# Optimization experiments

Hardware: AMD Instinct MI355X
Metric: run time of the kernel (lower is better)

Reference implementation:

```python
import jax, jax.numpy as jnp
import numpy as np

N = 262144        # 64^3 grid unknowns
NNZ = 7 * N       # ~7-point stencil sparsity
BS = 32


def setup_inputs() -> dict:
    key = jax.random.key(0)
    k1, k2, k3, k4, k5 = jax.random.split(key, 5)
    y_pred = jax.random.normal(k1, (BS, N), dtype=jnp.float32)
    y_true = jax.random.normal(k2, (BS, N), dtype=jnp.float32)
    A_vals = jax.random.normal(k3, (NNZ,), dtype=jnp.float32)
    A_rows = jax.random.randint(k4, (NNZ,), 0, N, dtype=jnp.int32)
    A_cols = jax.random.randint(k5, (NNZ,), 0, N, dtype=jnp.int32)
    return {"y_pred": y_pred, "y_true": y_true, "A_vals": A_vals,
            "A_rows": A_rows, "A_cols": A_cols}


def reference(y_pred, y_true, A_vals, A_rows, A_cols):
    # YhatY[b] = <y_true[b], y_pred[b]>
    YhatY = jnp.sum(y_true * y_pred, axis=1)                      # (bs,)
    # Sparse matvec per batch: YhatAt = (A @ y_pred.T).T, COO form.
    # gathered[e, b] = A_vals[e] * y_pred[b, A_cols[e]]
    gathered = (y_pred[:, A_cols] * A_vals).T                     # (nnz, bs)
    YhatAt = jax.ops.segment_sum(gathered, A_rows, num_segments=N).T  # (bs, N)
    # YhatYhatAt[b] = <y_pred[b], A y_pred[b]>
    YhatYhatAt = jnp.sum(y_pred * YhatAt, axis=1)                 # (bs,)
    # diag(YhatY / YhatYhatAt) @ YhatAt == row-wise scale by alpha
    alpha = YhatY / YhatYhatAt                                    # (bs,)
    resid = y_true - alpha[:, None] * YhatAt                      # (bs, N)
    return jnp.mean(jnp.sum(resid * resid, axis=1))
```

## Files before the change

kernel.cpp:

```cpp
#include <hip/hip_runtime.h>

#define NGRID 262144
#define NNZ_C 1835008
#define TP    260


__global__ __launch_bounds__(256) void k_prep(
        const float* __restrict__ yp, const float* __restrict__ yt,
        float* __restrict__ yp_t, float* __restrict__ yt_t,
        float* __restrict__ yat_t) {
    __shared__ __align__(16) float T[32 * TP];
    const int tid = threadIdx.x;
    const int l = tid & 63, w = tid >> 6;
    const int fam = blockIdx.x >> 10;
    const size_t n0 = (size_t)(blockIdx.x & 1023) * 256;
    const float* src = fam ? yt : yp;
    #pragma unroll
    for (int s = 0; s < 8; ++s) {
        const int b = s * 4 + w;
        const float4 a = *(const float4*)(src + (size_t)b * NGRID + n0 + 4 * l);
        *(float4*)(&T[b * TP + 4 * l]) = a;
    }
    __syncthreads();
    float4* dst4 = (float4*)((fam ? yt_t : yp_t) + n0 * 32);
    float4* yat4 = (float4*)(yat_t + n0 * 32);
    #pragma unroll
    for (int q = 0; q < 8; ++q) {
        const int f = q * 256 + tid;
        const int n = f >> 3;
        const int bb = 4 * (f & 7);
        float4 v;
        v.x = T[(bb + 0) * TP + n];
        v.y = T[(bb + 1) * TP + n];
        v.z = T[(bb + 2) * TP + n];
        v.w = T[(bb + 3) * TP + n];
        dst4[f] = v;
        if (!fam) yat4[f] = make_float4(0.f, 0.f, 0.f, 0.f);
    }
}

__global__ void k_scatter(const float* __restrict__ vals,
                          const int* __restrict__ rows,
                          const int* __restrict__ cols,
                          const float* __restrict__ yp_t,
                          float* __restrict__ yat_t) {
    const size_t tid = (size_t)blockIdx.x * blockDim.x + threadIdx.x;
    const int b = (int)(tid & 31);
    const size_t e = tid >> 5;
    const float v = vals[e];
    const int r = rows[e];
    const int c = cols[e];
    const float x = yp_t[(size_t)c * 32 + b];
    atomicAdd(&yat_t[(size_t)r * 32 + b], v * x);
}

__global__ __launch_bounds__(256) void k_post(
        const float* __restrict__ yat_t, const float* __restrict__ yp_t,
        const float* __restrict__ yt_t, float* __restrict__ p2) {
    __shared__ float redA[5][1024];
    const int tid = threadIdx.x;
    const size_t base = (size_t)blockIdx.x * 1024;
    const float4* yat4 = (const float4*)yat_t;
    const float4* yp4 = (const float4*)yp_t;
    const float4* yt4 = (const float4*)yt_t;
    float c1[4] = {0,0,0,0}, c2[4] = {0,0,0,0}, c3[4] = {0,0,0,0};
    float tt[4] = {0,0,0,0}, sy[4] = {0,0,0,0};
    #pragma unroll
    for (int q = 0; q < 4; ++q) {
        const size_t f = base + q * 256 + tid;
        const float4 a = yat4[f];
        const float4 p = yp4[f];
        const float4 t = yt4[f];
        c1[0] = fmaf(p.x, a.x, c1[0]); c2[0] = fmaf(t.x, a.x, c2[0]);
        c3[0] = fmaf(a.x, a.x, c3[0]); tt[0] = fmaf(t.x, t.x, tt[0]);
        sy[0] = fmaf(t.x, p.x, sy[0]);
        c1[1] = fmaf(p.y, a.y, c1[1]); c2[1] = fmaf(t.y, a.y, c2[1]);
        c3[1] = fmaf(a.y, a.y, c3[1]); tt[1] = fmaf(t.y, t.y, tt[1]);
        sy[1] = fmaf(t.y, p.y, sy[1]);
        c1[2] = fmaf(p.z, a.z, c1[2]); c2[2] = fmaf(t.z, a.z, c2[2]);
        c3[2] = fmaf(a.z, a.z, c3[2]); tt[2] = fmaf(t.z, t.z, tt[2]);
        sy[2] = fmaf(t.z, p.z, sy[2]);
        c1[3] = fmaf(p.w, a.w, c1[3]); c2[3] = fmaf(t.w, a.w, c2[3]);
        c3[3] = fmaf(a.w, a.w, c3[3]); tt[3] = fmaf(t.w, t.w, tt[3]);
        sy[3] = fmaf(t.w, p.w, sy[3]);
    }
    #pragma unroll
    for (int k = 0; k < 4; ++k) {
        redA[0][4 * tid + k] = c1[k];
        redA[1][4 * tid + k] = c2[k];
        redA[2][4 * tid + k] = c3[k];
        redA[3][4 * tid + k] = tt[k];
        redA[4][4 * tid + k] = sy[k];
    }
    __syncthreads();
    if (tid < 32) {
        #pragma unroll
        for (int s = 0; s < 5; ++s) {
            float acc = 0.f;
            #pragma unroll
            for (int j = 0; j < 32; ++j) acc += redA[s][tid + 32 * j];
            p2[blockIdx.x * 160 + s * 32 + tid] = acc;
        }
    }
}

__global__ __launch_bounds__(256) void k_finish1(
        const float* __restrict__ p2, float* __restrict__ pr2) {
    const int tid = threadIdx.x, g = blockIdx.x;
    if (tid < 160) {
        float acc = 0.f;
        #pragma unroll
        for (int j = 0; j < 32; ++j) acc += p2[(size_t)(g * 32 + j) * 160 + tid];
        pr2[g * 160 + tid] = acc;
    }
}

__global__ __launch_bounds__(256) void k_finish2(
        const float* __restrict__ pr2, float* __restrict__ out) {
    __shared__ float tot[160];
    __shared__ float lb[32];
    const int tid = threadIdx.x;
    if (tid < 160) {
        float acc = 0.f;
        #pragma unroll
        for (int j = 0; j < 64; ++j) acc += pr2[j * 160 + tid];
        tot[tid] = acc;
    }
    __syncthreads();
    if (tid < 32) {
        const float c1 = tot[0 + tid];
        const float c2 = tot[32 + tid];
        const float c3 = tot[64 + tid];
        const float stt = tot[96 + tid];
        const float sty = tot[128 + tid];
        const float a = sty / c1;
        lb[tid] = fmaf(a * a, c3, fmaf(-2.f * a, c2, stt));
    }
    __syncthreads();
    if (tid == 0) {
        float s = 0.f;
        #pragma unroll
        for (int i = 0; i < 32; ++i) s += lb[i];
        out[0] = s * (1.0f / 32.0f);
    }
}

extern "C" void kernel_launch(void* const* d_in, const int* in_sizes, int n_in,
                              void* d_out, int out_size, void* d_ws, size_t ws_size,
                              hipStream_t stream) {
    const float* yp = (const float*)d_in[0];
    const float* yt = (const float*)d_in[1];
    const float* Av = (const float*)d_in[2];
    const int*   Ar = (const int*)d_in[3];
    const int*   Ac = (const int*)d_in[4];
    float* out = (float*)d_out;

    float* ws    = (float*)d_ws;
    float* yp_t  = ws;
    float* yat_t = yp_t + (size_t)NGRID * 32;
    float* yt_t  = yat_t + (size_t)NGRID * 32;
    float* p2    = yt_t + (size_t)NGRID * 32;
    float* pr2   = p2 + 2048 * 160;

    k_prep<<<2048, 256, 0, stream>>>(yp, yt, yp_t, yt_t, yat_t);
    k_scatter<<<(NNZ_C * 32) / 256, 256, 0, stream>>>(Av, Ar, Ac, yp_t, yat_t);
    k_post<<<2048, 256, 0, stream>>>(yat_t, yp_t, yt_t, p2);
    k_finish1<<<64, 256, 0, stream>>>(p2, pr2);
    k_finish2<<<1, 256, 0, stream>>>(pr2, out);
}
```

Before: 330.7 us.

## Replace atomic COO scatter with per-call CSR build and row-gather SpMM

Each call now converts the COO matrix to CSR with a two-pass bucket sort: a coarse 1024-bucket histogram, scan and reorder, then a per-bucket sort into rows. A gather kernel then computes each row's sparse product for all 32 batches without atomics and fuses the dot-product reductions. This removes the yat_t buffer, its zeroing, and the 58M global float atomics. In exchange it adds several sorting kernels with atomics on the cursor and in shared memory, and a serial single-block scan. The gather loop is latency-bound, with two lanes per batch per row.

Result: slower. 360.3 us (+9.0%).

```diff
diff --git a/kernel.cpp b/kernel.cpp
--- a/kernel.cpp
+++ b/kernel.cpp
@@ -2,18 +2,23 @@
 
 #define NGRID 262144
 #define NNZ_C 1835008
+#define NBKT  1024
 #define TP    260
 
 
 __global__ __launch_bounds__(256) void k_prep(
         const float* __restrict__ yp, const float* __restrict__ yt,
         float* __restrict__ yp_t, float* __restrict__ yt_t,
-        float* __restrict__ yat_t) {
+        int* __restrict__ hist) {
     __shared__ __align__(16) float T[32 * TP];
     const int tid = threadIdx.x;
     const int l = tid & 63, w = tid >> 6;
     const int fam = blockIdx.x >> 10;
     const size_t n0 = (size_t)(blockIdx.x & 1023) * 256;
+    if (blockIdx.x == 0) {
+        #pragma unroll
+        for (int i = 0; i < 4; ++i) hist[i * 256 + tid] = 0;
+    }
     const float* src = fam ? yt : yp;
     #pragma unroll
     for (int s = 0; s < 8; ++s) {
@@ -23,7 +28,6 @@
     }
     __syncthreads();
     float4* dst4 = (float4*)((fam ? yt_t : yp_t) + n0 * 32);
-    float4* yat4 = (float4*)(yat_t + n0 * 32);
     #pragma unroll
     for (int q = 0; q < 8; ++q) {
         const int f = q * 256 + tid;
@@ -35,72 +39,149 @@
         v.z = T[(bb + 2) * TP + n];
         v.w = T[(bb + 3) * TP + n];
         dst4[f] = v;
-        if (!fam) yat4[f] = make_float4(0.f, 0.f, 0.f, 0.f);
-    }
-}
-
-__global__ void k_scatter(const float* __restrict__ vals,
-                          const int* __restrict__ rows,
-                          const int* __restrict__ cols,
-                          const float* __restrict__ yp_t,
-                          float* __restrict__ yat_t) {
-    const size_t tid = (size_t)blockIdx.x * blockDim.x + threadIdx.x;
-    const int b = (int)(tid & 31);
-    const size_t e = tid >> 5;
-    const float v = vals[e];
-    const int r = rows[e];
-    const int c = cols[e];
-    const float x = yp_t[(size_t)c * 32 + b];
-    atomicAdd(&yat_t[(size_t)r * 32 + b], v * x);
-}
-
-__global__ __launch_bounds__(256) void k_post(
-        const float* __restrict__ yat_t, const float* __restrict__ yp_t,
+    }
+}
+
+__global__ __launch_bounds__(256) void k_hist(const int* __restrict__ rows,
+                                              int* __restrict__ hist) {
+    __shared__ int h[NBKT];
+    const int tid = threadIdx.x;
+    for (int i = tid; i < NBKT; i += 256) h[i] = 0;
+    __syncthreads();
+    const int chunk = NNZ_C / 512;
+    const size_t e0 = (size_t)blockIdx.x * chunk;
+    for (int i = tid; i < chunk; i += 256) atomicAdd(&h[rows[e0 + i] >> 8], 1);
+    __syncthreads();
+    for (int i = tid; i < NBKT; i += 256)
+        if (h[i]) atomicAdd(&hist[i], h[i]);
+}
+
+__global__ __launch_bounds__(1024) void k_scan(const int* __restrict__ hist,
+                                               int* __restrict__ base,
+                                               int* __restrict__ cursor) {
+    __shared__ int s[2][NBKT];
+    const int tid = threadIdx.x;
+    const int v = hist[tid];
+    s[0][tid] = v;
+    __syncthreads();
+    int p = 0;
+    for (int off = 1; off < NBKT; off <<= 1) {
+        int t = s[p][tid];
+        if (tid >= off) t += s[p][tid - off];
+        s[1 ^ p][tid] = t;
+        __syncthreads();
+        p ^= 1;
+    }
+    const int excl = s[p][tid] - v;
+    base[tid] = excl;
+    cursor[tid] = excl;
+    if (tid == 0) base[NBKT] = NNZ_C;
+}
+
+__global__ __launch_bounds__(256) void k_reorder(
+        const int* __restrict__ rows, const int* __restrict__ cols,
+        const float* __restrict__ vals, int* __restrict__ cursor,
+        int* __restrict__ rc_out, float* __restrict__ v_out) {
+    __shared__ int h[NBKT];
+    __shared__ int bl[NBKT];
+    const int tid = threadIdx.x;
+    for (int i = tid; i < NBKT; i += 256) h[i] = 0;
+    __syncthreads();
+    const int chunk = NNZ_C / 256;
+    const size_t e0 = (size_t)blockIdx.x * chunk;
+    for (int i = tid; i < chunk; i += 256) atomicAdd(&h[rows[e0 + i] >> 8], 1);
+    __syncthreads();
+    for (int i = tid; i < NBKT; i += 256) {
+        const int c = h[i];
+        bl[i] = c ? atomicAdd(&cursor[i], c) : 0;
+        h[i] = 0;
+    }
+    __syncthreads();
+    for (int i = tid; i < chunk; i += 256) {
+        const int r = rows[e0 + i];
+        const int bk = r >> 8;
+        const int off = atomicAdd(&h[bk], 1);
+        const int pos = bl[bk] + off;
+        rc_out[pos] = ((r & 255) << 24) | cols[e0 + i];
+        v_out[pos] = vals[e0 + i];
+    }
+}
+
+__global__ __launch_bounds__(256) void k_reorder2(
+        const int* __restrict__ rc1, const float* __restrict__ v1,
+        const int* __restrict__ base, int* __restrict__ cols_s,
+        float* __restrict__ vals_s, int* __restrict__ row_ptr) {
+    __shared__ int s[2][256];
+    __shared__ int cur[256];
+    const int tid = threadIdx.x;
+    const int k = blockIdx.x;
+    const int start = base[k], end = base[k + 1];
+    s[0][tid] = 0;
+    __syncthreads();
+    for (int i = start + tid; i < end; i += 256)
+        atomicAdd(&s[0][((unsigned)rc1[i]) >> 24], 1);
+    __syncthreads();
+    const int v = s[0][tid];
+    int p = 0;
+    for (int off = 1; off < 256; off <<= 1) {
+        int t = s[p][tid];
+        if (tid >= off) t += s[p][tid - off];
+        s[1 ^ p][tid] = t;
+        __syncthreads();
+        p ^= 1;
+    }
+    const int excl = s[p][tid] - v;
+    row_ptr[k * 256 + tid] = start + excl;
+    cur[tid] = excl;
+    __syncthreads();
+    for (int i = start + tid; i < end; i += 256) {
+        const int rc = rc1[i];
+        const int r8 = (int)(((unsigned)rc) >> 24);
+        const int off = atomicAdd(&cur[r8], 1);
+        cols_s[start + off] = rc & 0x3FFFF;
+        vals_s[start + off] = v1[i];
+    }
+    if (k == NBKT - 1 && tid == 0) row_ptr[NGRID] = NNZ_C;
+}
+
+__global__ __launch_bounds__(256) void k_gather(
+        const int* __restrict__ cols_s, const float* __restrict__ vals_s,
+        const int* __restrict__ row_ptr, const float* __restrict__ yp_t,
         const float* __restrict__ yt_t, float* __restrict__ p2) {
-    __shared__ float redA[5][1024];
-    const int tid = threadIdx.x;
-    const size_t base = (size_t)blockIdx.x * 1024;
-    const float4* yat4 = (const float4*)yat_t;
-    const float4* yp4 = (const float4*)yp_t;
-    const float4* yt4 = (const float4*)yt_t;
-    float c1[4] = {0,0,0,0}, c2[4] = {0,0,0,0}, c3[4] = {0,0,0,0};
-    float tt[4] = {0,0,0,0}, sy[4] = {0,0,0,0};
-    #pragma unroll
-    for (int q = 0; q < 4; ++q) {
-        const size_t f = base + q * 256 + tid;
-        const float4 a = yat4[f];
-        const float4 p = yp4[f];
-        const float4 t = yt4[f];
-        c1[0] = fmaf(p.x, a.x, c1[0]); c2[0] = fmaf(t.x, a.x, c2[0]);
-        c3[0] = fmaf(a.x, a.x, c3[0]); tt[0] = fmaf(t.x, t.x, tt[0]);
-        sy[0] = fmaf(t.x, p.x, sy[0]);
-        c1[1] = fmaf(p.y, a.y, c1[1]); c2[1] = fmaf(t.y, a.y, c2[1]);
-        c3[1] = fmaf(a.y, a.y, c3[1]); tt[1] = fmaf(t.y, t.y, tt[1]);
-        sy[1] = fmaf(t.y, p.y, sy[1]);
-        c1[2] = fmaf(p.z, a.z, c1[2]); c2[2] = fmaf(t.z, a.z, c2[2]);
-        c3[2] = fmaf(a.z, a.z, c3[2]); tt[2] = fmaf(t.z, t.z, tt[2]);
-        sy[2] = fmaf(t.z, p.z, sy[2]);
-        c1[3] = fmaf(p.w, a.w, c1[3]); c2[3] = fmaf(t.w, a.w, c2[3]);
-        c3[3] = fmaf(a.w, a.w, c3[3]); tt[3] = fmaf(t.w, t.w, tt[3]);
-        sy[3] = fmaf(t.w, p.w, sy[3]);
-    }
-    #pragma unroll
-    for (int k = 0; k < 4; ++k) {
-        redA[0][4 * tid + k] = c1[k];
-        redA[1][4 * tid + k] = c2[k];
-        redA[2][4 * tid + k] = c3[k];
-        redA[3][4 * tid + k] = tt[k];
-        redA[4][4 * tid + k] = sy[k];
-    }
-    __syncthreads();
-    if (tid < 32) {
-        #pragma unroll
-        for (int s = 0; s < 5; ++s) {
-            float acc = 0.f;
-            #pragma unroll
-            for (int j = 0; j < 32; ++j) acc += redA[s][tid + 32 * j];
-            p2[blockIdx.x * 160 + s * 32 + tid] = acc;
+    __shared__ float R[4][5][32];
+    const int tid = threadIdx.x;
+    const int l = tid & 63, w = tid >> 6;
+    const int b = l & 31, j = l >> 5;
+    float C1 = 0.f, C2 = 0.f, C3 = 0.f, TT = 0.f, SY = 0.f;
+    const int r0 = blockIdx.x * 64 + w * 16;
+    for (int i = 0; i < 16; ++i) {
+        const int r = r0 + i;
+        const int s = row_ptr[r], e = row_ptr[r + 1];
+        float acc = 0.f;
+        for (int idx = s + j; idx < e; idx += 2) {
+            const int c = cols_s[idx];
+            const float v = vals_s[idx];
+            acc = fmaf(v, yp_t[(size_t)c * 32 + b], acc);
         }
+        acc += __shfl_down(acc, 32);
+        const float ypr = yp_t[(size_t)r * 32 + b];
+        const float ytr = yt_t[(size_t)r * 32 + b];
+        if (j == 0) {
+            C1 = fmaf(acc, ypr, C1);
+            C2 = fmaf(acc, ytr, C2);
+            C3 = fmaf(acc, acc, C3);
+        } else {
+            TT = fmaf(ytr, ytr, TT);
+            SY = fmaf(ytr, ypr, SY);
+        }
+    }
+    if (j == 0) { R[w][0][b] = C1; R[w][1][b] = C2; R[w][2][b] = C3; }
+    else        { R[w][3][b] = TT; R[w][4][b] = SY; }
+    __syncthreads();
+    if (tid < 160) {
+        const int s5 = tid >> 5, bb = tid & 31;
+        p2[blockIdx.x * 160 + tid] =
+            R[0][s5][bb] + R[1][s5][bb] + R[2][s5][bb] + R[3][s5][bb];
     }
 }
 
@@ -110,7 +191,7 @@
     if (tid < 160) {
         float acc = 0.f;
         #pragma unroll
-        for (int j = 0; j < 32; ++j) acc += p2[(size_t)(g * 32 + j) * 160 + tid];
+        for (int j = 0; j < 64; ++j) acc += p2[(size_t)(g * 64 + j) * 160 + tid];
         pr2[g * 160 + tid] = acc;
     }
 }
@@ -155,16 +236,26 @@
     const int*   Ac = (const int*)d_in[4];
     float* out = (float*)d_out;
 
-    float* ws    = (float*)d_ws;
-    float* yp_t  = ws;
-    float* yat_t = yp_t + (size_t)NGRID * 32;
-    float* yt_t  = yat_t + (size_t)NGRID * 32;
-    float* p2    = yt_t + (size_t)NGRID * 32;
-    float* pr2   = p2 + 2048 * 160;
-
-    k_prep<<<2048, 256, 0, stream>>>(yp, yt, yp_t, yt_t, yat_t);
-    k_scatter<<<(NNZ_C * 32) / 256, 256, 0, stream>>>(Av, Ar, Ac, yp_t, yat_t);
-    k_post<<<2048, 256, 0, stream>>>(yat_t, yp_t, yt_t, p2);
+    float* ws     = (float*)d_ws;
+    float* yp_t   = ws;
+    float* yt_t   = yp_t + (size_t)NGRID * 32;
+    int*   rc1    = (int*)(yt_t + (size_t)NGRID * 32);
+    float* v1     = (float*)(rc1 + NNZ_C);
+    int*   colss  = (int*)(v1 + NNZ_C);
+    float* valss  = (float*)(colss + NNZ_C);
+    int*   hist   = (int*)(valss + NNZ_C);
+    int*   basep  = hist + NBKT;
+    int*   cursor = basep + NBKT + 1;
+    int*   rowptr = cursor + NBKT;
+    float* p2     = (float*)(rowptr + NGRID + 1);
+    float* pr2    = p2 + 4096 * 160;
+
+    k_prep<<<2048, 256, 0, stream>>>(yp, yt, yp_t, yt_t, hist);
+    k_hist<<<512, 256, 0, stream>>>(Ar, hist);
+    k_scan<<<1, 1024, 0, stream>>>(hist, basep, cursor);
+    k_reorder<<<256, 256, 0, stream>>>(Ar, Ac, Av, cursor, rc1, v1);
+    k_reorder2<<<NBKT, 256, 0, stream>>>(rc1, v1, basep, colss, valss, rowptr);
+    k_gather<<<NGRID / 64, 256, 0, stream>>>(colss, valss, rowptr, yp_t, yt_t, p2);
     k_finish1<<<64, 256, 0, stream>>>(p2, pr2);
     k_finish2<<<1, 256, 0, stream>>>(pr2, out);
 }
```
